# Kernel optimization log

Hardware: AMD Instinct MI355X
Metric: run time of the kernel (lower is better)

Reference implementation:

```python
import jax, jax.numpy as jnp
import numpy as np

N = 50000      # nodes
E = 800000     # edges
IN_DIM = 128
HID = 16       # per-head hidden dim (layer1)
HEADS = 8
OUT_DIM = 32   # layer2 output dim (1 head)
NEG_SLOPE = 0.2  # GAT-paper LeakyReLU slope


def _gat_layer(x, W, a_src, a_dst, src, dst, num_nodes):
    """One multi-head GAT layer.
    x: [N, Fin]; W: [Fin, H*D]; a_src/a_dst: [H, D]; src/dst: [E].
    Returns [N, H, D].
    """
    H, D = a_src.shape
    z = (x @ W).reshape(num_nodes, H, D)            # [N, H, D]
    # edge attention logits: attn_fc([z_src || z_dst]) split into two dots
    e_s = jnp.einsum('nhd,hd->nh', z, a_src)        # [N, H]
    e_d = jnp.einsum('nhd,hd->nh', z, a_dst)        # [N, H]
    e = e_s[src] + e_d[dst]                          # [E, H]
    e = jnp.where(e >= 0, e, NEG_SLOPE * e)          # leaky_relu
    # softmax over incoming edges of each destination node
    m = jax.ops.segment_max(e, dst, num_segments=num_nodes)   # [N, H]
    ex = jnp.exp(e - m[dst])                                   # [E, H]
    s = jax.ops.segment_sum(ex, dst, num_segments=num_nodes)  # [N, H]
    alpha = ex / s[dst]                                        # [E, H]
    msg = alpha[:, :, None] * z[src]                            # [E, H, D]
    return jax.ops.segment_sum(msg, dst, num_segments=num_nodes)  # [N, H, D]


def setup_inputs() -> dict:
    key = jax.random.key(0)
    ks = jax.random.split(key, 9)
    h = jax.random.normal(ks[0], (N, IN_DIM), dtype=jnp.float32)
    src = jax.random.randint(ks[1], (E,), 0, N, dtype=jnp.int32)
    dst = jax.random.randint(ks[2], (E,), 0, N, dtype=jnp.int32)
    sc1 = 1.0 / np.sqrt(IN_DIM)
    W1 = jax.random.normal(ks[3], (IN_DIM, HEADS * HID), dtype=jnp.float32) * sc1
    a1_src = jax.random.normal(ks[4], (HEADS, HID), dtype=jnp.float32) * 0.1
    a1_dst = jax.random.normal(ks[5], (HEADS, HID), dtype=jnp.float32) * 0.1
    sc2 = 1.0 / np.sqrt(HEADS * HID)
    W2 = jax.random.normal(ks[6], (HEADS * HID, OUT_DIM), dtype=jnp.float32) * sc2
    a2_src = jax.random.normal(ks[7], (1, OUT_DIM), dtype=jnp.float32) * 0.1
    a2_dst = jax.random.normal(ks[8], (1, OUT_DIM), dtype=jnp.float32) * 0.1
    return {"h": h, "W1": W1, "a1_src": a1_src, "a1_dst": a1_dst,
            "W2": W2, "a2_src": a2_src, "a2_dst": a2_dst,
            "src": src, "dst": dst}


def reference(h, W1, a1_src, a1_dst, W2, a2_src, a2_dst, src, dst):
    # layer1: multi-head, concat heads -> [N, HEADS*HID]
    h1 = _gat_layer(h, W1, a1_src, a1_dst, src, dst, N).reshape(N, HEADS * HID)
    h1 = jax.nn.elu(h1)
    # layer2: single head -> [N, OUT_DIM]
    out = _gat_layer(h1, W2, a2_src, a2_dst, src, dst, N).reshape(N, OUT_DIM)
    return out
```

## Files before the change

### kernel.cpp

```cpp
#include <hip/hip_runtime.h>
#include <hip/hip_fp16.h>
#include <math.h>

#define NN 50000
#define EE 800000
#define FIN 128
#define F1  128
#define NH  8
#define DH  16
#define F2  32
#define SLOPE 0.2f
#define LOG2E 1.44269504f

#define EB 4096
#define NBLK ((EE + EB - 1) / EB)
#define BK  391
#define SEGCAP 4096
#define PREPB 80
#define GEMM1B ((NN + 63) / 64)

typedef _Float16 f16x8 __attribute__((ext_vector_type(8)));
typedef float    f32x4 __attribute__((ext_vector_type(4)));

__global__ __launch_bounds__(256) void k1_hist_prep(const int* __restrict__ dst,
        const float* __restrict__ W1, const float* __restrict__ W2,
        __half* __restrict__ wt1, __half* __restrict__ wt2, int* __restrict__ hist) {
    int tid = threadIdx.x;
    if (blockIdx.x < NBLK) {
        __shared__ int lc[BK];
        for (int i = tid; i < BK; i += 256) lc[i] = 0;
        __syncthreads();
        int base = blockIdx.x * EB;
        int end = base + EB; if (end > EE) end = EE;
        for (int i = base + tid; i < end; i += 256)
            atomicAdd(&lc[dst[i] >> 7], 1);
        __syncthreads();
        for (int i = tid; i < BK; i += 256)
            if (lc[i]) atomicAdd(&hist[i], lc[i]);
    } else {
        int gidx = (blockIdx.x - NBLK) * 256 + tid;
        if (gidx < FIN * F1) {
            int n = gidx >> 7, k = gidx & 127;
            wt1[gidx] = __float2half(W1[k * F1 + n]);
        } else {
            int t2 = gidx - FIN * F1;
            if (t2 < F2 * FIN) {
                int n = t2 >> 7, k = t2 & 127;
                wt2[t2] = __float2half(W2[k * F2 + n]);
            }
        }
    }
}

extern __shared__ char smem_k2[];
__global__ __launch_bounds__(256) void k2_split_gemm1(const int* __restrict__ src,
        const int* __restrict__ dst, const int* __restrict__ hist, int* __restrict__ cursor,
        unsigned int* __restrict__ sorted,
        const float* __restrict__ h, const __half* __restrict__ wt1,
        const float* __restrict__ a1s, const float* __restrict__ a1d,
        __half* __restrict__ z1h, float* __restrict__ es1x, float* __restrict__ ed1x) {
    int tid = threadIdx.x;
    if (blockIdx.x < NBLK) {
        unsigned int*   recs = (unsigned int*)smem_k2;
        unsigned short* rbk  = (unsigned short*)(smem_k2 + 16384);
        int* lc    = (int*)(smem_k2 + 24576);
        int* lofs  = (int*)(smem_k2 + 26624);
        int* lcur  = (int*)(smem_k2 + 28672);
        int* delta = (int*)(smem_k2 + 30720);
        int* bscan = (int*)(smem_k2 + 32768);
        int* sh    = (int*)(smem_k2 + 34816);
        for (int i = tid; i < 512; i += 256) lc[i] = 0;
        __syncthreads();
        int base = blockIdx.x * EB;
        int cnt = EE - base; if (cnt > EB) cnt = EB;
        unsigned int myrec[16];
        #pragma unroll
        for (int k = 0; k < 16; ++k) {
            int i = base + tid + k * 256;
            myrec[k] = 0xFFFFFFFFu;
            if (i - base < cnt) {
                unsigned int d = (unsigned int)dst[i];
                myrec[k] = (d << 16) | (unsigned int)src[i];
                atomicAdd(&lc[d >> 7], 1);
            }
        }
        __syncthreads();
        int a0 = lc[2 * tid], a1 = lc[2 * tid + 1];
        int tsum = a0 + a1;
        sh[tid] = tsum;
        __syncthreads();
        for (int off = 1; off < 256; off <<= 1) {
            int t = (tid >= off) ? sh[tid - off] : 0;
            __syncthreads(); sh[tid] += t; __syncthreads();
        }
        int ex = sh[tid] - tsum;
        lofs[2 * tid] = ex;
        lofs[2 * tid + 1] = ex + a0;
        __syncthreads();
        int h0 = hist[2 * tid], h1 = hist[2 * tid + 1];
        int hsum = h0 + h1;
        sh[tid] = hsum;
        __syncthreads();
        for (int off = 1; off < 256; off <<= 1) {
            int t = (tid >= off) ? sh[tid - off] : 0;
            __syncthreads(); sh[tid] += t; __syncthreads();
        }
        int hex = sh[tid] - hsum;
        bscan[2 * tid] = hex;
        bscan[2 * tid + 1] = hex + h0;
        __syncthreads();
        for (int b = tid; b < BK; b += 256) {
            int c = lc[b];
            lcur[b] = lofs[b];
            if (c) {
                int g = atomicAdd(&cursor[b], c);
                delta[b] = bscan[b] + g - lofs[b];
            }
        }
        __syncthreads();
        #pragma unroll
        for (int k = 0; k < 16; ++k) {
            if (myrec[k] != 0xFFFFFFFFu) {
                int b = (int)(myrec[k] >> 23);
                int pos = atomicAdd(&lcur[b], 1);
                recs[pos] = myrec[k];
                rbk[pos] = (unsigned short)b;
            }
        }
        __syncthreads();
        for (int s = tid; s < cnt; s += 256)
            sorted[s + delta[rbk[s]]] = recs[s];
    } else {
        __half* hs  = (__half*)smem_k2;
        __half* wls = (__half*)(smem_k2 + 17408);
        for (int c = tid; c < 2048; c += 256) {
            int row = c >> 4, ch = c & 15;
            *(float4*)&wls[row * 136 + ch * 8] = *(const float4*)&wt1[row * 128 + ch * 8];
        }
        int rowBase = (blockIdx.x - NBLK) * 64;
        for (int idx4 = tid; idx4 < 64 * 32; idx4 += 256) {
            int r = idx4 >> 5, cc = (idx4 & 31) * 4;
            int n = rowBase + r;
            float4 v = (n < NN) ? *(const float4*)&h[(size_t)n * FIN + cc] : make_float4(0, 0, 0, 0);
            union { __half2 h2[2]; int2 i; } u;
            u.h2[0] = __floats2half2_rn(v.x, v.y);
            u.h2[1] = __floats2half2_rn(v.z, v.w);
            *(int2*)&hs[r * 136 + cc] = u.i;
        }
        __syncthreads();
        int l = tid & 63, w = tid >> 6;
        int q = l >> 4, cl = l & 15;
        int m0 = w * 16;
        float as[8], ad[8];
        #pragma unroll
        for (int t = 0; t < 8; ++t) { as[t] = a1s[t * DH + cl]; ad[t] = a1d[t * DH + cl]; }
        f32x4 acc[8];
        #pragma unroll
        for (int t = 0; t < 8; ++t) acc[t] = (f32x4){0.f, 0.f, 0.f, 0.f};
        const __half* ap = &hs[(m0 + cl) * 136 + q * 8];
        const __half* bp = &wls[cl * 136 + q * 8];
        #pragma unroll
        for (int k0 = 0; k0 < 128; k0 += 32) {
            f16x8 af = *(const f16x8*)(ap + k0);
            #pragma unroll
            for (int t = 0; t < 8; ++t) {
                f16x8 bf = *(const f16x8*)(bp + t * 16 * 136 + k0);
                acc[t] = __builtin_amdgcn_mfma_f32_16x16x32_f16(af, bf, acc[t], 0, 0, 0);
            }
        }
        #pragma unroll
        for (int t = 0; t < 8; ++t) {
            #pragma unroll
            for (int reg = 0; reg < 4; ++reg) {
                int row = rowBase + m0 + q * 4 + reg;
                float z = acc[t][reg];
                float s = z * as[t], d = z * ad[t];
                s += __shfl_xor(s, 1, 64); d += __shfl_xor(d, 1, 64);
                s += __shfl_xor(s, 2, 64); d += __shfl_xor(d, 2, 64);
                s += __shfl_xor(s, 4, 64); d += __shfl_xor(d, 4, 64);
                s += __shfl_xor(s, 8, 64); d += __shfl_xor(d, 8, 64);
                if (row < NN) {
                    z1h[(size_t)row * F1 + t * 16 + cl] = __float2half(z);
                    if (cl == 0) {
                        es1x[row * NH + t] = s * LOG2E;
                        ed1x[row * NH + t] = d * LOG2E;
                    }
                }
            }
        }
    }
}

__global__ __launch_bounds__(256) void csrbuild_kernel(const int* __restrict__ hist,
        const unsigned int* __restrict__ sorted, unsigned short* __restrict__ csr,
        int* __restrict__ row_ptr) {
    __shared__ unsigned int recs[SEGCAP];
    __shared__ unsigned short csr_sh[SEGCAP];
    __shared__ int ncnt[128], ncur[128];
    __shared__ int sh[256];
    __shared__ int bscan[512];
    int b = blockIdx.x;
    int tid = threadIdx.x;
    int h0 = hist[2 * tid], h1 = hist[2 * tid + 1];
    int hsum = h0 + h1;
    sh[tid] = hsum;
    if (tid < 128) ncnt[tid] = 0;
    __syncthreads();
    for (int off = 1; off < 256; off <<= 1) {
        int t = (tid >= off) ? sh[tid - off] : 0;
        __syncthreads(); sh[tid] += t; __syncthreads();
    }
    int hex = sh[tid] - hsum;
    bscan[2 * tid] = hex;
    bscan[2 * tid + 1] = hex + h0;
    __syncthreads();
    int s0 = bscan[b], s1 = bscan[b + 1];
    int cnt = s1 - s0; if (cnt > SEGCAP) cnt = SEGCAP;
    for (int i = tid; i < cnt; i += 256) {
        unsigned int r = sorted[s0 + i];
        recs[i] = r;
        atomicAdd(&ncnt[(r >> 16) & 127], 1);
    }
    __syncthreads();
    int v = (tid < 128) ? ncnt[tid] : 0;
    sh[tid] = v;
    __syncthreads();
    for (int off = 1; off < 256; off <<= 1) {
        int t = (tid >= off) ? sh[tid - off] : 0;
        __syncthreads(); sh[tid] += t; __syncthreads();
    }
    int ex = sh[tid] - v;
    if (tid < 128) {
        ncur[tid] = ex;
        int node = b * 128 + tid;
        if (node < NN) row_ptr[node] = s0 + ex;
    }
    if (b == BK - 1 && tid == 0) row_ptr[NN] = EE;
    __syncthreads();
    for (int i = tid; i < cnt; i += 256) {
        unsigned int r = recs[i];
        int local = (r >> 16) & 127;
        int p = atomicAdd(&ncur[local], 1);
        csr_sh[p] = (unsigned short)(r & 0xFFFFu);
    }
    __syncthreads();
    for (int i = tid; i < cnt; i += 256)
        csr[s0 + i] = csr_sh[i];
}

__global__ __launch_bounds__(256) void gemm2_kernel(const __half* __restrict__ h1h,
        const __half* __restrict__ wt2, const float* __restrict__ a2s, const float* __restrict__ a2d,
        __half* __restrict__ z2h, float* __restrict__ es2x, float* __restrict__ ed2x) {
    __shared__ alignas(16) __half hs[64 * 136];
    __shared__ alignas(16) __half wls[32 * 136];
    int tid = threadIdx.x;
    for (int c = tid; c < 512; c += 256) {
        int row = c >> 4, ch = c & 15;
        *(float4*)&wls[row * 136 + ch * 8] = *(const float4*)&wt2[row * 128 + ch * 8];
    }
    int rowBase = blockIdx.x * 64;
    for (int idx8 = tid; idx8 < 64 * 16; idx8 += 256) {
        int r = idx8 >> 4, cc = (idx8 & 15) * 8;
        int n = rowBase + r;
        float4 v = make_float4(0, 0, 0, 0);
        if (n < NN) v = *(const float4*)&h1h[(size_t)n * FIN + cc];
        *(float4*)&hs[r * 136 + cc] = v;
    }
    __syncthreads();
    int l = tid & 63, w = tid >> 6;
    int q = l >> 4, cl = l & 15;
    int m0 = w * 16;
    float as0 = a2s[cl], as1 = a2s[16 + cl];
    float ad0 = a2d[cl], ad1 = a2d[16 + cl];
    f32x4 acc[2];
    acc[0] = (f32x4){0.f, 0.f, 0.f, 0.f};
    acc[1] = (f32x4){0.f, 0.f, 0.f, 0.f};
    const __half* ap = &hs[(m0 + cl) * 136 + q * 8];
    const __half* bp = &wls[cl * 136 + q * 8];
    #pragma unroll
    for (int k0 = 0; k0 < 128; k0 += 32) {
        f16x8 af = *(const f16x8*)(ap + k0);
        #pragma unroll
        for (int t = 0; t < 2; ++t) {
            f16x8 bf = *(const f16x8*)(bp + t * 16 * 136 + k0);
            acc[t] = __builtin_amdgcn_mfma_f32_16x16x32_f16(af, bf, acc[t], 0, 0, 0);
        }
    }
    #pragma unroll
    for (int reg = 0; reg < 4; ++reg) {
        int row = rowBase + m0 + q * 4 + reg;
        float s = acc[0][reg] * as0 + acc[1][reg] * as1;
        float d = acc[0][reg] * ad0 + acc[1][reg] * ad1;
        s += __shfl_xor(s, 1, 64); d += __shfl_xor(d, 1, 64);
        s += __shfl_xor(s, 2, 64); d += __shfl_xor(d, 2, 64);
        s += __shfl_xor(s, 4, 64); d += __shfl_xor(d, 4, 64);
        s += __shfl_xor(s, 8, 64); d += __shfl_xor(d, 8, 64);
        if (row < NN) {
            z2h[(size_t)row * F2 + cl]      = __float2half(acc[0][reg]);
            z2h[(size_t)row * F2 + 16 + cl] = __float2half(acc[1][reg]);
            if (cl == 0) {
                es2x[row] = s * LOG2E;
                ed2x[row] = d * LOG2E;
            }
        }
    }
}

__global__ __launch_bounds__(256) void attn1_kernel(const int* __restrict__ row_ptr,
        const unsigned short* __restrict__ csr, const __half* __restrict__ z1h,
        const float* __restrict__ es, const float* __restrict__ ed,
        __half* __restrict__ h1h) {
    int gt = blockIdx.x * 256 + threadIdx.x;
    int n = gt >> 4;
    int j = gt & 15;
    int hl = j >> 1;
    if (n >= NN) return;
    int b0 = row_ptr[n];
    int cnt = row_ptr[n + 1] - b0;
    float edn = ed[n * NH + hl];
    float acc[8] = {0.f, 0.f, 0.f, 0.f, 0.f, 0.f, 0.f, 0.f};
    float ws = 0.f;
    int i = 0;
    for (; i + 4 <= cnt; i += 4) {
        int s0 = csr[b0 + i], s1 = csr[b0 + i + 1], s2 = csr[b0 + i + 2], s3 = csr[b0 + i + 3];
        float e0 = es[s0 * NH + hl] + edn;
        float e1 = es[s1 * NH + hl] + edn;
        float e2 = es[s2 * NH + hl] + edn;
        float e3 = es[s3 * NH + hl] + edn;
        union { float4 f; __half2 h2[4]; } u0, u1, u2, u3;
        u0.f = *(const float4*)&z1h[(size_t)s0 * F1 + j * 8];
        u1.f = *(const float4*)&z1h[(size_t)s1 * F1 + j * 8];
        u2.f = *(const float4*)&z1h[(size_t)s2 * F1 + j * 8];
        u3.f = *(const float4*)&z1h[(size_t)s3 * F1 + j * 8];
        float w0 = exp2f(e0 >= 0.f ? e0 : SLOPE * e0);
        float w1 = exp2f(e1 >= 0.f ? e1 : SLOPE * e1);
        float w2 = exp2f(e2 >= 0.f ? e2 : SLOPE * e2);
        float w3 = exp2f(e3 >= 0.f ? e3 : SLOPE * e3);
        ws += (w0 + w1) + (w2 + w3);
        #pragma unroll
        for (int t = 0; t < 4; ++t) {
            float2 v0 = __half22float2(u0.h2[t]);
            float2 v1 = __half22float2(u1.h2[t]);
            float2 v2 = __half22float2(u2.h2[t]);
            float2 v3 = __half22float2(u3.h2[t]);
            acc[2*t]   = fmaf(w0, v0.x, fmaf(w1, v1.x, fmaf(w2, v2.x, fmaf(w3, v3.x, acc[2*t]))));
            acc[2*t+1] = fmaf(w0, v0.y, fmaf(w1, v1.y, fmaf(w2, v2.y, fmaf(w3, v3.y, acc[2*t+1]))));
        }
    }
    for (; i < cnt; ++i) {
        int s = csr[b0 + i];
        float e = es[s * NH + hl] + edn;
        float wv = exp2f(e >= 0.f ? e : SLOPE * e);
        ws += wv;
        union { float4 f; __half2 h2[4]; } u;
        u.f = *(const float4*)&z1h[(size_t)s * F1 + j * 8];
        #pragma unroll
        for (int t = 0; t < 4; ++t) {
            float2 v = __half22float2(u.h2[t]);
            acc[2*t]   = fmaf(wv, v.x, acc[2*t]);
            acc[2*t+1] = fmaf(wv, v.y, acc[2*t+1]);
        }
    }
    float rs = ws > 0.f ? 1.0f / ws : 0.f;
    union { float4 f; __half2 h2[4]; } p;
    #pragma unroll
    for (int t = 0; t < 4; ++t) {
        float x0 = acc[2*t] * rs, x1 = acc[2*t+1] * rs;
        x0 = x0 > 0.f ? x0 : __expf(x0) - 1.0f;
        x1 = x1 > 0.f ? x1 : __expf(x1) - 1.0f;
        p.h2[t] = __floats2half2_rn(x0, x1);
    }
    *(float4*)&h1h[(size_t)n * F1 + j * 8] = p.f;
}

__global__ __launch_bounds__(256) void attn2_kernel(const int* __restrict__ row_ptr,
        const unsigned short* __restrict__ csr, const __half* __restrict__ z2h,
        const float* __restrict__ es, const float* __restrict__ ed,
        float* __restrict__ out) {
    int gt = blockIdx.x * 256 + threadIdx.x;
    int n = gt >> 2;
    int j = gt & 3;
    if (n >= NN) return;
    int b0 = row_ptr[n];
    int cnt = row_ptr[n + 1] - b0;
    float edn = ed[n];
    float acc[8] = {0.f, 0.f, 0.f, 0.f, 0.f, 0.f, 0.f, 0.f};
    float ws = 0.f;
    int i = 0;
    for (; i + 4 <= cnt; i += 4) {
        int s0 = csr[b0 + i], s1 = csr[b0 + i + 1], s2 = csr[b0 + i + 2], s3 = csr[b0 + i + 3];
        float e0 = es[s0] + edn;
        float e1 = es[s1] + edn;
        float e2 = es[s2] + edn;
        float e3 = es[s3] + edn;
        union { float4 f; __half2 h2[4]; } u0, u1, u2, u3;
        u0.f = *(const float4*)&z2h[(size_t)s0 * F2 + j * 8];
        u1.f = *(const float4*)&z2h[(size_t)s1 * F2 + j * 8];
        u2.f = *(const float4*)&z2h[(size_t)s2 * F2 + j * 8];
        u3.f = *(const float4*)&z2h[(size_t)s3 * F2 + j * 8];
        float w0 = exp2f(e0 >= 0.f ? e0 : SLOPE * e0);
        float w1 = exp2f(e1 >= 0.f ? e1 : SLOPE * e1);
        float w2 = exp2f(e2 >= 0.f ? e2 : SLOPE * e2);
        float w3 = exp2f(e3 >= 0.f ? e3 : SLOPE * e3);
        ws += (w0 + w1) + (w2 + w3);
        #pragma unroll
        for (int t = 0; t < 4; ++t) {
            float2 v0 = __half22float2(u0.h2[t]);
            float2 v1 = __half22float2(u1.h2[t]);
            float2 v2 = __half22float2(u2.h2[t]);
            float2 v3 = __half22float2(u3.h2[t]);
            acc[2*t]   = fmaf(w0, v0.x, fmaf(w1, v1.x, fmaf(w2, v2.x, fmaf(w3, v3.x, acc[2*t]))));
            acc[2*t+1] = fmaf(w0, v0.y, fmaf(w1, v1.y, fmaf(w2, v2.y, fmaf(w3, v3.y, acc[2*t+1]))));
        }
    }
    for (; i < cnt; ++i) {
        int s = csr[b0 + i];
        float e = es[s] + edn;
        float wv = exp2f(e >= 0.f ? e : SLOPE * e);
        ws += wv;
        union { float4 f; __half2 h2[4]; } u;
        u.f = *(const float4*)&z2h[(size_t)s * F2 + j * 8];
        #pragma unroll
        for (int t = 0; t < 4; ++t) {
            float2 v = __half22float2(u.h2[t]);
            acc[2*t]   = fmaf(wv, v.x, acc[2*t]);
            acc[2*t+1] = fmaf(wv, v.y, acc[2*t+1]);
        }
    }
    float rs = ws > 0.f ? 1.0f / ws : 0.f;
    float* op = &out[(size_t)n * F2 + j * 8];
    *(float4*)&op[0] = make_float4(acc[0]*rs, acc[1]*rs, acc[2]*rs, acc[3]*rs);
    *(float4*)&op[4] = make_float4(acc[4]*rs, acc[5]*rs, acc[6]*rs, acc[7]*rs);
}

extern "C" void kernel_launch(void* const* d_in, const int* in_sizes, int n_in,
                              void* d_out, int out_size, void* d_ws, size_t ws_size,
                              hipStream_t stream) {
    const float* h   = (const float*)d_in[0];
    const float* W1  = (const float*)d_in[1];
    const float* a1s = (const float*)d_in[2];
    const float* a1d = (const float*)d_in[3];
    const float* W2  = (const float*)d_in[4];
    const float* a2s = (const float*)d_in[5];
    const float* a2d = (const float*)d_in[6];
    const int*   src = (const int*)d_in[7];
    const int*   dst = (const int*)d_in[8];
    float* out = (float*)d_out;

    int* ip      = (int*)d_ws;
    int* hist    = ip;
    int* cursor  = hist + 512;
    int* row_ptr = cursor + 512;
    unsigned int* sorted = (unsigned int*)(row_ptr + NN + 8);
    unsigned short* csr16 = (unsigned short*)(sorted + EE);
    float* es1x = (float*)(csr16 + EE);
    float* ed1x = es1x + (size_t)NN * NH;
    float* es2x = ed1x + (size_t)NN * NH;
    float* ed2x = es2x + NN;
    __half* z1h = (__half*)(ed2x + NN);
    __half* h1h = z1h + (size_t)NN * F1;
    __half* z2h = h1h + (size_t)NN * F1;
    __half* wt1 = z2h + (size_t)NN * F2;
    __half* wt2 = wt1 + FIN * F1;

    hipMemsetAsync(hist, 0, 1024 * sizeof(int), stream);

    k1_hist_prep<<<NBLK + PREPB, 256, 0, stream>>>(dst, W1, W2, wt1, wt2, hist);
    k2_split_gemm1<<<NBLK + GEMM1B, 256, 52224, stream>>>(src, dst, hist, cursor, sorted,
                                                          h, wt1, a1s, a1d, z1h, es1x, ed1x);
    csrbuild_kernel<<<BK, 256, 0, stream>>>(hist, sorted, csr16, row_ptr);
    attn1_kernel<<<(NN * 16 + 255) / 256, 256, 0, stream>>>(row_ptr, csr16, z1h, es1x, ed1x, h1h);
    gemm2_kernel<<<GEMM1B, 256, 0, stream>>>(h1h, wt2, a2s, a2d, z2h, es2x, ed2x);
    attn2_kernel<<<(NN * 4 + 255) / 256, 256, 0, stream>>>(row_ptr, csr16, z2h, es2x, ed2x, out);
}
```

Before: 199.4 us.

## Fuse layer-1 attention aggregation into layer-2 GEMM kernel via shared memory

Merges the layer-1 attention/aggregation kernel with the layer-2 projection GEMM, so each block computes 64 nodes' ELU-activated h1 rows directly into shared memory and then runs the MFMA GEMM on them. This removes the global h1 intermediate buffer, its write and read traffic, and one kernel launch. In exchange, the gather work runs on far fewer blocks, each doing four serial passes. That reduces parallelism and latency hiding for the irregular neighbor gathers.

```diff
diff --git a/kernel.cpp b/kernel.cpp
--- a/kernel.cpp
+++ b/kernel.cpp
@@ -248,7 +248,9 @@
         csr[s0 + i] = csr_sh[i];
 }
 
-__global__ __launch_bounds__(256) void gemm2_kernel(const __half* __restrict__ h1h,
+__global__ __launch_bounds__(256) void attn1_gemm2_kernel(const int* __restrict__ row_ptr,
+        const unsigned short* __restrict__ csr, const __half* __restrict__ z1h,
+        const float* __restrict__ es, const float* __restrict__ ed,
         const __half* __restrict__ wt2, const float* __restrict__ a2s, const float* __restrict__ a2d,
         __half* __restrict__ z2h, float* __restrict__ es2x, float* __restrict__ ed2x) {
     __shared__ alignas(16) __half hs[64 * 136];
@@ -259,12 +261,72 @@
         *(float4*)&wls[row * 136 + ch * 8] = *(const float4*)&wt2[row * 128 + ch * 8];
     }
     int rowBase = blockIdx.x * 64;
-    for (int idx8 = tid; idx8 < 64 * 16; idx8 += 256) {
-        int r = idx8 >> 4, cc = (idx8 & 15) * 8;
-        int n = rowBase + r;
-        float4 v = make_float4(0, 0, 0, 0);
-        if (n < NN) v = *(const float4*)&h1h[(size_t)n * FIN + cc];
-        *(float4*)&hs[r * 136 + cc] = v;
+    int j = tid & 15;
+    int hl = j >> 1;
+    #pragma unroll
+    for (int pass = 0; pass < 4; ++pass) {
+        int lr = pass * 16 + (tid >> 4);
+        int n = rowBase + lr;
+        union { float4 f; __half2 h2[4]; } p;
+        if (n < NN) {
+            int b0 = row_ptr[n];
+            int cnt = row_ptr[n + 1] - b0;
+            float edn = ed[n * NH + hl];
+            float acc[8] = {0.f, 0.f, 0.f, 0.f, 0.f, 0.f, 0.f, 0.f};
+            float ws = 0.f;
+            int i = 0;
+            for (; i + 4 <= cnt; i += 4) {
+                int s0 = csr[b0 + i], s1 = csr[b0 + i + 1], s2 = csr[b0 + i + 2], s3 = csr[b0 + i + 3];
+                float e0 = es[s0 * NH + hl] + edn;
+                float e1 = es[s1 * NH + hl] + edn;
+                float e2 = es[s2 * NH + hl] + edn;
+                float e3 = es[s3 * NH + hl] + edn;
+                union { float4 f; __half2 h2[4]; } u0, u1, u2, u3;
+                u0.f = *(const float4*)&z1h[(size_t)s0 * F1 + j * 8];
+                u1.f = *(const float4*)&z1h[(size_t)s1 * F1 + j * 8];
+                u2.f = *(const float4*)&z1h[(size_t)s2 * F1 + j * 8];
+                u3.f = *(const float4*)&z1h[(size_t)s3 * F1 + j * 8];
+                float w0 = exp2f(e0 >= 0.f ? e0 : SLOPE * e0);
+                float w1 = exp2f(e1 >= 0.f ? e1 : SLOPE * e1);
+                float w2 = exp2f(e2 >= 0.f ? e2 : SLOPE * e2);
+                float w3 = exp2f(e3 >= 0.f ? e3 : SLOPE * e3);
+                ws += (w0 + w1) + (w2 + w3);
+                #pragma unroll
+                for (int t = 0; t < 4; ++t) {
+                    float2 v0 = __half22float2(u0.h2[t]);
+                    float2 v1 = __half22float2(u1.h2[t]);
+                    float2 v2 = __half22float2(u2.h2[t]);
+                    float2 v3 = __half22float2(u3.h2[t]);
+                    acc[2*t]   = fmaf(w0, v0.x, fmaf(w1, v1.x, fmaf(w2, v2.x, fmaf(w3, v3.x, acc[2*t]))));
+                    acc[2*t+1] = fmaf(w0, v0.y, fmaf(w1, v1.y, fmaf(w2, v2.y, fmaf(w3, v3.y, acc[2*t+1]))));
+                }
+            }
+            for (; i < cnt; ++i) {
+                int s = csr[b0 + i];
+                float e = es[s * NH + hl] + edn;
+                float wv = exp2f(e >= 0.f ? e : SLOPE * e);
+                ws += wv;
+                union { float4 f; __half2 h2[4]; } u;
+                u.f = *(const float4*)&z1h[(size_t)s * F1 + j * 8];
+                #pragma unroll
+                for (int t = 0; t < 4; ++t) {
+                    float2 v = __half22float2(u.h2[t]);
+                    acc[2*t]   = fmaf(wv, v.x, acc[2*t]);
+                    acc[2*t+1] = fmaf(wv, v.y, acc[2*t+1]);
+                }
+            }
+            float rs = ws > 0.f ? 1.0f / ws : 0.f;
+            #pragma unroll
+            for (int t = 0; t < 4; ++t) {
+                float x0 = acc[2*t] * rs, x1 = acc[2*t+1] * rs;
+                x0 = x0 > 0.f ? x0 : __expf(x0) - 1.0f;
+                x1 = x1 > 0.f ? x1 : __expf(x1) - 1.0f;
+                p.h2[t] = __floats2half2_rn(x0, x1);
+            }
+        } else {
+            p.f = make_float4(0.f, 0.f, 0.f, 0.f);
+        }
+        *(float4*)&hs[lr * 136 + j * 8] = p.f;
     }
     __syncthreads();
     int l = tid & 63, w = tid >> 6;
@@ -272,9 +334,9 @@
     int m0 = w * 16;
     float as0 = a2s[cl], as1 = a2s[16 + cl];
     float ad0 = a2d[cl], ad1 = a2d[16 + cl];
-    f32x4 acc[2];
-    acc[0] = (f32x4){0.f, 0.f, 0.f, 0.f};
-    acc[1] = (f32x4){0.f, 0.f, 0.f, 0.f};
+    f32x4 acc2[2];
+    acc2[0] = (f32x4){0.f, 0.f, 0.f, 0.f};
+    acc2[1] = (f32x4){0.f, 0.f, 0.f, 0.f};
     const __half* ap = &hs[(m0 + cl) * 136 + q * 8];
     const __half* bp = &wls[cl * 136 + q * 8];
     #pragma unroll
@@ -283,94 +345,27 @@
         #pragma unroll
         for (int t = 0; t < 2; ++t) {
             f16x8 bf = *(const f16x8*)(bp + t * 16 * 136 + k0);
-            acc[t] = __builtin_amdgcn_mfma_f32_16x16x32_f16(af, bf, acc[t], 0, 0, 0);
+            acc2[t] = __builtin_amdgcn_mfma_f32_16x16x32_f16(af, bf, acc2[t], 0, 0, 0);
         }
     }
     #pragma unroll
     for (int reg = 0; reg < 4; ++reg) {
         int row = rowBase + m0 + q * 4 + reg;
-        float s = acc[0][reg] * as0 + acc[1][reg] * as1;
-        float d = acc[0][reg] * ad0 + acc[1][reg] * ad1;
+        float s = acc2[0][reg] * as0 + acc2[1][reg] * as1;
+        float d = acc2[0][reg] * ad0 + acc2[1][reg] * ad1;
         s += __shfl_xor(s, 1, 64); d += __shfl_xor(d, 1, 64);
         s += __shfl_xor(s, 2, 64); d += __shfl_xor(d, 2, 64);
         s += __shfl_xor(s, 4, 64); d += __shfl_xor(d, 4, 64);
         s += __shfl_xor(s, 8, 64); d += __shfl_xor(d, 8, 64);
         if (row < NN) {
-            z2h[(size_t)row * F2 + cl]      = __float2half(acc[0][reg]);
-            z2h[(size_t)row * F2 + 16 + cl] = __float2half(acc[1][reg]);
+            z2h[(size_t)row * F2 + cl]      = __float2half(acc2[0][reg]);
+            z2h[(size_t)row * F2 + 16 + cl] = __float2half(acc2[1][reg]);
             if (cl == 0) {
                 es2x[row] = s * LOG2E;
                 ed2x[row] = d * LOG2E;
             }
         }
     }
-}
-
-__global__ __launch_bounds__(256) void attn1_kernel(const int* __restrict__ row_ptr,
-        const unsigned short* __restrict__ csr, const __half* __restrict__ z1h,
-        const float* __restrict__ es, const float* __restrict__ ed,
-        __half* __restrict__ h1h) {
-    int gt = blockIdx.x * 256 + threadIdx.x;
-    int n = gt >> 4;
-    int j = gt & 15;
-    int hl = j >> 1;
-    if (n >= NN) return;
-    int b0 = row_ptr[n];
-    int cnt = row_ptr[n + 1] - b0;
-    float edn = ed[n * NH + hl];
-    float acc[8] = {0.f, 0.f, 0.f, 0.f, 0.f, 0.f, 0.f, 0.f};
-    float ws = 0.f;
-    int i = 0;
-    for (; i + 4 <= cnt; i += 4) {
-        int s0 = csr[b0 + i], s1 = csr[b0 + i + 1], s2 = csr[b0 + i + 2], s3 = csr[b0 + i + 3];
-        float e0 = es[s0 * NH + hl] + edn;
-        float e1 = es[s1 * NH + hl] + edn;
-        float e2 = es[s2 * NH + hl] + edn;
-        float e3 = es[s3 * NH + hl] + edn;
-        union { float4 f; __half2 h2[4]; } u0, u1, u2, u3;
-        u0.f = *(const float4*)&z1h[(size_t)s0 * F1 + j * 8];
-        u1.f = *(const float4*)&z1h[(size_t)s1 * F1 + j * 8];
-        u2.f = *(const float4*)&z1h[(size_t)s2 * F1 + j * 8];
-        u3.f = *(const float4*)&z1h[(size_t)s3 * F1 + j * 8];
-        float w0 = exp2f(e0 >= 0.f ? e0 : SLOPE * e0);
-        float w1 = exp2f(e1 >= 0.f ? e1 : SLOPE * e1);
-        float w2 = exp2f(e2 >= 0.f ? e2 : SLOPE * e2);
-        float w3 = exp2f(e3 >= 0.f ? e3 : SLOPE * e3);
-        ws += (w0 + w1) + (w2 + w3);
-        #pragma unroll
-        for (int t = 0; t < 4; ++t) {
-            float2 v0 = __half22float2(u0.h2[t]);
-            float2 v1 = __half22float2(u1.h2[t]);
-            float2 v2 = __half22float2(u2.h2[t]);
-            float2 v3 = __half22float2(u3.h2[t]);
-            acc[2*t]   = fmaf(w0, v0.x, fmaf(w1, v1.x, fmaf(w2, v2.x, fmaf(w3, v3.x, acc[2*t]))));
-            acc[2*t+1] = fmaf(w0, v0.y, fmaf(w1, v1.y, fmaf(w2, v2.y, fmaf(w3, v3.y, acc[2*t+1]))));
-        }
-    }
-    for (; i < cnt; ++i) {
-        int s = csr[b0 + i];
-        float e = es[s * NH + hl] + edn;
-        float wv = exp2f(e >= 0.f ? e : SLOPE * e);
-        ws += wv;
-        union { float4 f; __half2 h2[4]; } u;
-        u.f = *(const float4*)&z1h[(size_t)s * F1 + j * 8];
-        #pragma unroll
-        for (int t = 0; t < 4; ++t) {
-            float2 v = __half22float2(u.h2[t]);
-            acc[2*t]   = fmaf(wv, v.x, acc[2*t]);
-            acc[2*t+1] = fmaf(wv, v.y, acc[2*t+1]);
-        }
-    }
-    float rs = ws > 0.f ? 1.0f / ws : 0.f;
-    union { float4 f; __half2 h2[4]; } p;
-    #pragma unroll
-    for (int t = 0; t < 4; ++t) {
-        float x0 = acc[2*t] * rs, x1 = acc[2*t+1] * rs;
-        x0 = x0 > 0.f ? x0 : __expf(x0) - 1.0f;
-        x1 = x1 > 0.f ? x1 : __expf(x1) - 1.0f;
-        p.h2[t] = __floats2half2_rn(x0, x1);
-    }
-    *(float4*)&h1h[(size_t)n * F1 + j * 8] = p.f;
 }
 
 __global__ __launch_bounds__(256) void attn2_kernel(const int* __restrict__ row_ptr,
@@ -458,8 +453,7 @@
     float* es2x = ed1x + (size_t)NN * NH;
     float* ed2x = es2x + NN;
     __half* z1h = (__half*)(ed2x + NN);
-    __half* h1h = z1h + (size_t)NN * F1;
-    __half* z2h = h1h + (size_t)NN * F1;
+    __half* z2h = z1h + (size_t)NN * F1;
     __half* wt1 = z2h + (size_t)NN * F2;
     __half* wt2 = wt1 + FIN * F1;
 
@@ -469,7 +463,7 @@
     k2_split_gemm1<<<NBLK + GEMM1B, 256, 52224, stream>>>(src, dst, hist, cursor, sorted,
                                                           h, wt1, a1s, a1d, z1h, es1x, ed1x);
     csrbuild_kernel<<<BK, 256, 0, stream>>>(hist, sorted, csr16, row_ptr);
-    attn1_kernel<<<(NN * 16 + 255) / 256, 256, 0, stream>>>(row_ptr, csr16, z1h, es1x, ed1x, h1h);
-    gemm2_kernel<<<GEMM1B, 256, 0, stream>>>(h1h, wt2, a2s, a2d, z2h, es2x, ed2x);
+    attn1_gemm2_kernel<<<GEMM1B, 256, 0, stream>>>(row_ptr, csr16, z1h, es1x, ed1x,
+                                                   wt2, a2s, a2d, z2h, es2x, ed2x);
     attn2_kernel<<<(NN * 4 + 255) / 256, 256, 0, stream>>>(row_ptr, csr16, z2h, es2x, ed2x, out);
 }
```

Result: no change. 196.0 us (-1.7%).
